# Optimization experiments

Measured on AMD Instinct MI355X. Metric: run time of the kernel, lower is better.

The kernel has to match this reference:

```python
import jax, jax.numpy as jnp
import numpy as np

G = 16          # avg_pool_output_size (grid side after adaptive pool)
PATCH = 2       # patch_size
HIDDEN = 256
NOUT = 128


def setup_inputs() -> dict:
    key = jax.random.key(0)
    ks = jax.random.split(key, 7)
    B, C, H, W = 8, 32, 32, 32
    D = C * PATCH * PATCH + 2          # 130 (patch pixels + 2 coords)
    IN0 = 2 * D                        # 260 (pair concat)
    s = 0.02
    return {
        "x": jax.random.normal(ks[0], (B, C, H, W), jnp.float32),
        "W0": jax.random.normal(ks[1], (IN0, HIDDEN), jnp.float32) * s,
        "b0": jax.random.normal(ks[2], (HIDDEN,), jnp.float32) * s,
        "W1": jax.random.normal(ks[3], (HIDDEN, HIDDEN), jnp.float32) * s,
        "b1": jax.random.normal(ks[4], (HIDDEN,), jnp.float32) * s,
        "Wout": jax.random.normal(ks[5], (HIDDEN, NOUT), jnp.float32) * s,
        "bout": jax.random.normal(ks[6], (NOUT,), jnp.float32) * s,
    }


def _patch_node_features(x):
    """x: [B,C,H,W] -> node features [B, P, C*p^2 + 2] (patch pixels + coords)."""
    b, c, h, w = x.shape
    # adaptive avg pool to GxG (evenly divisible case == block mean)
    pooled = x.reshape(b, c, G, h // G, G, w // G).mean(axis=(3, 5))  # [B,C,G,G]
    flat = pooled.reshape(b, c, G * G)
    Pg = G - PATCH + 1                          # patches per side (15)
    P = Pg * Pg                                 # 225 nodes
    ri = jnp.arange(Pg)
    ki = jnp.arange(PATCH)
    # flat pixel index (r+ki)*G + (q+kj), patch order row-major, pixel order row-major
    row = (ri[:, None, None, None] + ki[None, None, :, None])  # [Pg,1,p,1]
    col = (ri[None, :, None, None] + ki[None, None, None, :])  # [1,Pg,1,p]
    pix = (row * G + col).reshape(P, PATCH * PATCH)            # [P, p^2]
    feats = flat[:, :, pix]                                    # [B,C,P,p^2]
    # torch: [b,c,P,p2] -> permute -> [b,c,p2,P] -> reshape [b,c*p2,P] -> [b,P,c*p2]
    feats = feats.transpose(0, 2, 1, 3).reshape(b, P, c * PATCH * PATCH)
    # spatial coordinates: (x=col, y=row) centered by int(sqrt(P)/2)
    cx = jnp.broadcast_to(jnp.arange(Pg)[None, :], (Pg, Pg))
    cy = jnp.broadcast_to(jnp.arange(Pg)[:, None], (Pg, Pg))
    coord = jnp.stack([cx, cy], axis=-1).reshape(P, 2).astype(feats.dtype) - (Pg // 2)
    coord = jnp.broadcast_to(coord[None], (b, P, 2))
    return jnp.concatenate([feats, coord], axis=2)             # [B,P,D]


def reference(x, W0, b0, W1, b1, Wout, bout):
    feats = _patch_node_features(x)          # [B,P,D]
    b, P, D = feats.shape
    # pair tensor: cat([x_i, x_j]) with x_i[b,i,j]=feats[b,j], x_j[b,i,j]=feats[b,i]
    pair = jnp.concatenate([
        jnp.broadcast_to(feats[:, None, :, :], (b, P, P, D)),
        jnp.broadcast_to(feats[:, :, None, :], (b, P, P, D)),
    ], axis=-1).reshape(b, P * P, 2 * D)     # [B, P^2, 2D]
    out = jax.nn.leaky_relu(pair @ W0 + b0)  # [B,P^2,H]
    out = jax.nn.leaky_relu(out @ W1 + b1)
    out = out.mean(axis=1)                   # [B,H]
    return out @ Wout + bout                 # [B,NOUT]
```

## Files before the change

kernel.cpp:

```cpp
#include <hip/hip_runtime.h>
#include <hip/hip_bf16.h>
#include <stdint.h>

#define NB 8
#define NP 225
#define PGRID 15
#define DH 256
#define DIN 130

typedef _Float16 f16x8 __attribute__((ext_vector_type(8)));
typedef float    f32x4 __attribute__((ext_vector_type(4)));

static __device__ __forceinline__ float lrelu(float x) { return fmaxf(x, 0.01f * x); }

__global__ void prep_kernel(const float* __restrict__ x, const float* __restrict__ W0,
                            const float* __restrict__ b0, const float* __restrict__ W1,
                            _Float16* __restrict__ U, _Float16* __restrict__ V,
                            _Float16* __restrict__ W1F, float* __restrict__ accg) {
    int blk = blockIdx.x;
    if (blk >= 360) {
        int t = (blk - 360) * 256 + threadIdx.x;
        int slot = t >> 6, l = t & 63;
        int nf = slot >> 3, ks = slot & 7;
        int n = nf * 16 + (l & 15);
        int kb = l >> 4;
        f16x8 wv;
        #pragma unroll
        for (int e = 0; e < 8; ++e) {
            int k = ks * 32 + kb * 8 + e;
            wv[e] = (_Float16)W1[k * DH + n];
        }
        reinterpret_cast<f16x8*>(W1F)[t] = wv;
        return;
    }
    int bb = blk / 45;
    int p0 = (blk % 45) * 5;
    if (blk % 45 == 0) accg[bb * DH + threadIdx.x] = 0.0f;
    __shared__ float fl[5][DIN];
    int t = threadIdx.x;
    for (int idx = t; idx < 5 * DIN; idx += 256) {
        int pp = idx / DIN, f = idx % DIN;
        int p = p0 + pp;
        int r = p / PGRID, c = p % PGRID;
        float val;
        if (f < 128) {
            int ch = f >> 2, q = f & 3, ki = q >> 1, kj = q & 1;
            int R = r + ki, C = c + kj;
            const float* xp = x + (((size_t)bb * 32 + ch) * 32 + 2 * R) * 32 + 2 * C;
            val = 0.25f * (xp[0] + xp[1] + xp[32] + xp[33]);
        } else {
            val = (f == 128) ? (float)(c - 7) : (float)(r - 7);
        }
        fl[pp][f] = val;
    }
    __syncthreads();
    int n = t;
    float u[5] = {0, 0, 0, 0, 0}, v[5] = {0, 0, 0, 0, 0};
    for (int k = 0; k < DIN; ++k) {
        float wa = W0[k * DH + n];
        float wb = W0[(DIN + k) * DH + n];
        #pragma unroll
        for (int pp = 0; pp < 5; ++pp) {
            float f = fl[pp][k];
            u[pp] = fmaf(f, wa, u[pp]);
            v[pp] = fmaf(f, wb, v[pp]);
        }
    }
    float bb0 = b0[n];
    #pragma unroll
    for (int pp = 0; pp < 5; ++pp) {
        size_t base = ((size_t)bb * NP + p0 + pp) * DH + n;
        U[base] = (_Float16)(u[pp] + bb0);
        V[base] = (_Float16)v[pp];
    }
}

__global__ __launch_bounds__(256, 2) void main_kernel(
        const _Float16* __restrict__ U, const _Float16* __restrict__ V,
        const _Float16* __restrict__ W1F, const float* __restrict__ b1,
        float* __restrict__ accg) {
    __shared__ f16x8 Af[2048];
    __shared__ _Float16 Upad[16 * 264];
    __shared__ _Float16 Vlds[28 * 256];
    const int JT = 15, CHUNKS = 9, TILESPC = 7;
    int blk = blockIdx.x;
    int bb = blk / (JT * CHUNKS);
    int rem = blk % (JT * CHUNKS);
    int jt = rem / CHUNKS, ch = rem % CHUNKS;
    int j0 = jt * 16;
    int tile0 = ch * TILESPC;
    int nt = min(TILESPC, 57 - tile0);
    int t = threadIdx.x, l = t & 63, w = t >> 6;

    {
        const _Float16* Vsrc = V + ((size_t)bb * NP + tile0 * 4) * DH;
        for (int q = w * 4; q < 14 && q < w * 4 + 4; ++q) {
            __builtin_amdgcn_global_load_lds(
                (const __attribute__((address_space(1))) void*)(Vsrc + q * 512 + (size_t)l * 8),
                (__attribute__((address_space(3))) void*)(&Vlds[q * 512]),
                16, 0, 0);
        }
    }
    {
        int jj = t >> 4, kk = (t & 15) * 16;
        int jc = j0 + jj; if (jc >= NP) jc = NP - 1;
        const f16x8* src = reinterpret_cast<const f16x8*>(U + ((size_t)bb * NP + jc) * DH + kk);
        *reinterpret_cast<f16x8*>(&Upad[jj * 264 + kk])     = src[0];
        *reinterpret_cast<f16x8*>(&Upad[jj * 264 + kk + 8]) = src[1];
    }
    f16x8 bv[4][8];
    const f16x8* Bp = reinterpret_cast<const f16x8*>(W1F);
    #pragma unroll
    for (int nf = 0; nf < 4; ++nf)
        #pragma unroll
        for (int ks = 0; ks < 8; ++ks)
            bv[nf][ks] = Bp[((w * 4 + nf) * 8 + ks) * 64 + l];
    float b1v[4];
    #pragma unroll
    for (int nf = 0; nf < 4; ++nf) b1v[nf] = b1[w * 64 + nf * 16 + (l & 15)];
    float psum[4] = {0.f, 0.f, 0.f, 0.f};
    int kb = l >> 4;
    const _Float16* Urow = &Upad[(l & 15) * 264 + kb * 8];
    __syncthreads();

    for (int itl = 0; itl < nt; ++itl) {
        #pragma unroll
        for (int nf = 0; nf < 4; ++nf)
            #pragma unroll
            for (int ks = 0; ks < 8; ++ks)
                asm volatile("" : "+v"(bv[nf][ks]));

        int i0 = (tile0 + itl) * 4;
        int vrow = itl * 4 + w;
        const f16x8* Vrow = reinterpret_cast<const f16x8*>(&Vlds[vrow * 256]);
        if (itl) __syncthreads();

        #pragma unroll
        for (int ks = 0; ks < 8; ++ks) {
            f16x8 uv = *reinterpret_cast<const f16x8*>(Urow + ks * 32);
            f16x8 vv = Vrow[ks * 4 + kb];
            f16x8 s  = uv + vv;
            f16x8 a  = __builtin_elementwise_max(s, s * (_Float16)0.01f);
            Af[(w * 8 + ks) * 64 + l] = a;
        }
        __syncthreads();

        f32x4 acc[4][4];
        #pragma unroll
        for (int mf = 0; mf < 4; ++mf)
            #pragma unroll
            for (int nf = 0; nf < 4; ++nf)
                acc[mf][nf] = (f32x4){b1v[nf], b1v[nf], b1v[nf], b1v[nf]};
        #pragma unroll
        for (int ks = 0; ks < 8; ++ks) {
            f16x8 av[4];
            #pragma unroll
            for (int mf = 0; mf < 4; ++mf) av[mf] = Af[(mf * 8 + ks) * 64 + l];
            #pragma unroll
            for (int mf = 0; mf < 4; ++mf)
                #pragma unroll
                for (int nf = 0; nf < 4; ++nf)
                    acc[mf][nf] = __builtin_amdgcn_mfma_f32_16x16x32_f16(
                        av[mf], bv[nf][ks], acc[mf][nf], 0, 0, 0);
        }

        int rowg = l >> 4;
        #pragma unroll
        for (int mf = 0; mf < 4; ++mf) {
            bool iv = (i0 + mf) < NP;
            #pragma unroll
            for (int r = 0; r < 4; ++r) {
                bool valid = iv && ((j0 + rowg * 4 + r) < NP);
                #pragma unroll
                for (int nf = 0; nf < 4; ++nf) {
                    float h = lrelu(acc[mf][nf][r]);
                    psum[nf] += valid ? h : 0.f;
                }
            }
        }
    }

    #pragma unroll
    for (int nf = 0; nf < 4; ++nf) {
        psum[nf] += __shfl_xor(psum[nf], 16);
        psum[nf] += __shfl_xor(psum[nf], 32);
    }
    if (l < 16) {
        #pragma unroll
        for (int nf = 0; nf < 4; ++nf)
            atomicAdd(&accg[bb * DH + w * 64 + nf * 16 + l], psum[nf]);
    }
}

__global__ void out_kernel(const float* __restrict__ accg, const float* __restrict__ Wout,
                           const float* __restrict__ bout, float* __restrict__ out) {
    int bb = blockIdx.x;
    int o = threadIdx.x;
    float s = 0.f;
    for (int n = 0; n < DH; ++n)
        s = fmaf(accg[bb * DH + n], Wout[n * 128 + o], s);
    out[bb * 128 + o] = s * (1.0f / 50625.0f) + bout[o];
}

extern "C" void kernel_launch(void* const* d_in, const int* in_sizes, int n_in,
                              void* d_out, int out_size, void* d_ws, size_t ws_size,
                              hipStream_t stream) {
    const float* x    = (const float*)d_in[0];
    const float* W0   = (const float*)d_in[1];
    const float* b0   = (const float*)d_in[2];
    const float* W1   = (const float*)d_in[3];
    const float* b1   = (const float*)d_in[4];
    const float* Wout = (const float*)d_in[5];
    const float* bout = (const float*)d_in[6];
    float* out = (float*)d_out;

    char* ws = (char*)d_ws;
    _Float16* U    = (_Float16*)(ws);
    _Float16* V    = (_Float16*)(ws + 921600);
    _Float16* W1F  = (_Float16*)(ws + 2 * 921600);
    float*    accg = (float*)(ws + 2 * 921600 + 131072);

    prep_kernel<<<392, 256, 0, stream>>>(x, W0, b0, W1, U, V, W1F, accg);
    main_kernel<<<NB * 15 * 9, 256, 0, stream>>>(U, V, W1F, b1, accg);
    out_kernel<<<NB, 128, 0, stream>>>(accg, Wout, bout, out);
}
```

Before: 86.00 us.

## Retile main kernel warps to 2x8 MFMA fragments with 128-column B halves

Changes the per-wave work split in the pairwise MLP kernel. Each wave previously covered all 4 M-fragments and a 64-column N slice; it now covers 2 M-fragments and a 128-column half. Each wave therefore keeps 8x8 W1 fragments in registers and does fewer LDS A-fragment reads per MFMA. This doubles the register footprint for B and accumulators, so launch bounds drop to 1 block per SM, which risks lower occupancy. The validity mask is also precomputed as a float multiplier and the per-fragment i check becomes a branch.

```diff
diff --git a/kernel.cpp b/kernel.cpp
--- a/kernel.cpp
+++ b/kernel.cpp
@@ -75,7 +75,7 @@
     }
 }
 
-__global__ __launch_bounds__(256, 2) void main_kernel(
+__global__ __launch_bounds__(256, 1) void main_kernel(
         const _Float16* __restrict__ U, const _Float16* __restrict__ V,
         const _Float16* __restrict__ W1F, const float* __restrict__ b1,
         float* __restrict__ accg) {
@@ -91,6 +91,7 @@
     int tile0 = ch * TILESPC;
     int nt = min(TILESPC, 57 - tile0);
     int t = threadIdx.x, l = t & 63, w = t >> 6;
+    int nhalf = w & 1, mhalf = w >> 1;
 
     {
         const _Float16* Vsrc = V + ((size_t)bb * NP + tile0 * 4) * DH;
@@ -108,31 +109,34 @@
         *reinterpret_cast<f16x8*>(&Upad[jj * 264 + kk])     = src[0];
         *reinterpret_cast<f16x8*>(&Upad[jj * 264 + kk + 8]) = src[1];
     }
-    f16x8 bv[4][8];
+    f16x8 bv[8][8];
     const f16x8* Bp = reinterpret_cast<const f16x8*>(W1F);
     #pragma unroll
-    for (int nf = 0; nf < 4; ++nf)
+    for (int nf = 0; nf < 8; ++nf)
         #pragma unroll
         for (int ks = 0; ks < 8; ++ks)
-            bv[nf][ks] = Bp[((w * 4 + nf) * 8 + ks) * 64 + l];
-    float b1v[4];
-    #pragma unroll
-    for (int nf = 0; nf < 4; ++nf) b1v[nf] = b1[w * 64 + nf * 16 + (l & 15)];
-    float psum[4] = {0.f, 0.f, 0.f, 0.f};
+            bv[nf][ks] = Bp[((nhalf * 8 + nf) * 8 + ks) * 64 + l];
+    float b1v[8];
+    #pragma unroll
+    for (int nf = 0; nf < 8; ++nf) b1v[nf] = b1[nhalf * 128 + nf * 16 + (l & 15)];
+    int rowg = l >> 4;
+    float jmask[4];
+    #pragma unroll
+    for (int r = 0; r < 4; ++r) jmask[r] = (j0 + rowg * 4 + r) < NP ? 1.0f : 0.0f;
+    float psum[8] = {0.f, 0.f, 0.f, 0.f, 0.f, 0.f, 0.f, 0.f};
     int kb = l >> 4;
     const _Float16* Urow = &Upad[(l & 15) * 264 + kb * 8];
     __syncthreads();
 
     for (int itl = 0; itl < nt; ++itl) {
         #pragma unroll
-        for (int nf = 0; nf < 4; ++nf)
+        for (int nf = 0; nf < 8; ++nf)
             #pragma unroll
             for (int ks = 0; ks < 8; ++ks)
                 asm volatile("" : "+v"(bv[nf][ks]));
 
         int i0 = (tile0 + itl) * 4;
-        int vrow = itl * 4 + w;
-        const f16x8* Vrow = reinterpret_cast<const f16x8*>(&Vlds[vrow * 256]);
+        const f16x8* Vrow = reinterpret_cast<const f16x8*>(&Vlds[(itl * 4 + w) * 256]);
         if (itl) __syncthreads();
 
         #pragma unroll
@@ -145,50 +149,51 @@
         }
         __syncthreads();
 
-        f32x4 acc[4][4];
-        #pragma unroll
-        for (int mf = 0; mf < 4; ++mf)
-            #pragma unroll
-            for (int nf = 0; nf < 4; ++nf)
-                acc[mf][nf] = (f32x4){b1v[nf], b1v[nf], b1v[nf], b1v[nf]};
+        f32x4 acc[2][8];
+        #pragma unroll
+        for (int m2 = 0; m2 < 2; ++m2)
+            #pragma unroll
+            for (int nf = 0; nf < 8; ++nf)
+                acc[m2][nf] = (f32x4){b1v[nf], b1v[nf], b1v[nf], b1v[nf]};
         #pragma unroll
         for (int ks = 0; ks < 8; ++ks) {
-            f16x8 av[4];
-            #pragma unroll
-            for (int mf = 0; mf < 4; ++mf) av[mf] = Af[(mf * 8 + ks) * 64 + l];
-            #pragma unroll
-            for (int mf = 0; mf < 4; ++mf)
+            f16x8 av[2];
+            #pragma unroll
+            for (int m2 = 0; m2 < 2; ++m2)
+                av[m2] = Af[((mhalf * 2 + m2) * 8 + ks) * 64 + l];
+            #pragma unroll
+            for (int m2 = 0; m2 < 2; ++m2)
                 #pragma unroll
-                for (int nf = 0; nf < 4; ++nf)
-                    acc[mf][nf] = __builtin_amdgcn_mfma_f32_16x16x32_f16(
-                        av[mf], bv[nf][ks], acc[mf][nf], 0, 0, 0);
-        }
-
-        int rowg = l >> 4;
-        #pragma unroll
-        for (int mf = 0; mf < 4; ++mf) {
-            bool iv = (i0 + mf) < NP;
-            #pragma unroll
-            for (int r = 0; r < 4; ++r) {
-                bool valid = iv && ((j0 + rowg * 4 + r) < NP);
+                for (int nf = 0; nf < 8; ++nf)
+                    acc[m2][nf] = __builtin_amdgcn_mfma_f32_16x16x32_f16(
+                        av[m2], bv[nf][ks], acc[m2][nf], 0, 0, 0);
+        }
+
+        #pragma unroll
+        for (int m2 = 0; m2 < 2; ++m2) {
+            if (i0 + mhalf * 2 + m2 < NP) {
                 #pragma unroll
-                for (int nf = 0; nf < 4; ++nf) {
-                    float h = lrelu(acc[mf][nf][r]);
-                    psum[nf] += valid ? h : 0.f;
+                for (int r = 0; r < 4; ++r) {
+                    #pragma unroll
+                    for (int nf = 0; nf < 8; ++nf) {
+                        float a = acc[m2][nf][r];
+                        float h = fmaxf(a, 0.01f * a);
+                        psum[nf] = fmaf(h, jmask[r], psum[nf]);
+                    }
                 }
             }
         }
     }
 
     #pragma unroll
-    for (int nf = 0; nf < 4; ++nf) {
+    for (int nf = 0; nf < 8; ++nf) {
         psum[nf] += __shfl_xor(psum[nf], 16);
         psum[nf] += __shfl_xor(psum[nf], 32);
     }
     if (l < 16) {
         #pragma unroll
-        for (int nf = 0; nf < 4; ++nf)
-            atomicAdd(&accg[bb * DH + w * 64 + nf * 16 + l], psum[nf]);
+        for (int nf = 0; nf < 8; ++nf)
+            atomicAdd(&accg[bb * DH + nhalf * 128 + nf * 16 + l], psum[nf]);
     }
 }
 
```

Result: slower. 130.4 us (+51.7%).
